# Performance work log

Hardware: AMD Instinct MI355X
Metric: run time of the kernel (lower is better)

## Reference

```python
import jax, jax.numpy as jnp
import numpy as np

C = 32        # channels after first 1x1 conv
HEADS = 4     # FuncSelfAttention heads ('channel' head split -> d = C // HEADS)


def setup_inputs() -> dict:
    key = jax.random.key(0)
    ks = jax.random.split(key, 8)
    B, H, W = 8, 512, 512
    s = 0.1
    return {
        "x": jax.random.normal(ks[0], (B, 1, H, W), jnp.float32),
        "n": 8,
        "m": 8,
        # Conv2d(1, C, kernel_size=1) == per-pixel linear 1->C
        "w1": jax.random.normal(ks[1], (C, 1), jnp.float32) * s,
        "b1": jax.random.normal(ks[2], (C,), jnp.float32) * s,
        # fused QKV projection over channels, bias=False
        "wqkv": jax.random.normal(ks[3], (3 * C, C), jnp.float32) * s,
        # output projection of the attention
        "wproj": jax.random.normal(ks[4], (C, C), jnp.float32) * s,
        "bproj": jax.random.normal(ks[5], (C,), jnp.float32) * s,
        # Conv2d(C, 1, kernel_size=1)
        "w2": jax.random.normal(ks[6], (1, C), jnp.float32) * s,
        "b2": jax.random.normal(ks[7], (1,), jnp.float32) * s,
    }


def reference(x, n, m, w1, b1, wqkv, wproj, bproj, w2, b2):
    B, _, H, W = x.shape
    d = C // HEADS
    hh, ww = H // n, W // m
    S, P = n * m, hh * ww  # subdomain tokens, quadrature points per token

    # 1x1 conv (pointwise linear over channel dim)
    h = jnp.einsum('oi,bihw->bohw', w1, x) + b1[None, :, None, None]

    # decompose2d: [B,C,H,W] -> [B, n*m, C, hh, ww] (flatten spatial per token)
    u = h.reshape(B, C, n, hh, m, ww).transpose(0, 2, 4, 1, 3, 5)
    u = u.reshape(B, S, C, P)

    # channel self-attention over subdomain functions
    qkv = jnp.einsum('oc,bscp->bsop', wqkv, u)          # [B,S,3C,P]
    q, k, v = jnp.split(qkv, 3, axis=2)
    q = q.reshape(B, S, HEADS, d, P)
    k = k.reshape(B, S, HEADS, d, P)
    v = v.reshape(B, S, HEADS, d, P)

    # L2 (quadrature-mean) inner product over points + head channels
    scale = 1.0 / (P * np.sqrt(d).astype(np.float32))
    scores = jnp.einsum('bihdp,bjhdp->bhij', q, k) * scale  # [B,H,S,S]
    attn = jax.nn.softmax(scores, axis=-1)
    o = jnp.einsum('bhij,bjhdp->bihdp', attn, v).reshape(B, S, C, P)
    o = jnp.einsum('oc,bscp->bsop', wproj, o) + bproj[None, None, :, None]

    # recompose2d: [B, n*m, C, hh, ww] -> [B, C, H, W]
    o = o.reshape(B, n, m, C, hh, ww).transpose(0, 3, 1, 4, 2, 5)
    o = o.reshape(B, C, H, W)

    # final 1x1 conv C -> 1
    out = jnp.einsum('oc,bchw->bohw', w2, o) + b2[None, :, None, None]
    return out
```

## Files before the change

kernel.cpp:

```cpp
#include <hip/hip_runtime.h>


#define CONST_OFF 0
#define SXP_OFF   16
#define WT_OFF    (16 + 128*64)
#define PART_OFF  (WT_OFF + 8*4096)

__global__ __launch_bounds__(256) void k1_gram(const float* __restrict__ x,
                                               float* __restrict__ ws)
{
    __shared__ float xs[64 * 68];
    int b = blockIdx.x >> 4, prg = blockIdx.x & 15;
    int t = threadIdx.x;
    const float* xb = x + (size_t)b * 262144;
    int tix = t & 15, tjx = t >> 4;

    float acc[4][4];
    #pragma unroll
    for (int u = 0; u < 4; ++u)
        #pragma unroll
        for (int v = 0; v < 4; ++v) acc[u][v] = 0.f;
    float tsum = 0.f;

    for (int it = 0; it < 4; ++it) {
        int pr = prg * 4 + it;
        __syncthreads();
        #pragma unroll
        for (int k = 0; k < 4; ++k) {
            int q = t + 256 * k;
            int tj = q >> 7, col4 = q & 127;
            float4 v = *(const float4*)(xb + (tj * 64 + pr) * 512 + col4 * 4);
            int token = tj * 8 + (col4 >> 4);
            *(float4*)(&xs[token * 68 + (col4 & 15) * 4]) = v;
        }
        __syncthreads();

        #pragma unroll 4
        for (int cq = 0; cq < 16; ++cq) {
            float4 a[4], bb[4];
            #pragma unroll
            for (int u = 0; u < 4; ++u)
                a[u] = *(const float4*)(&xs[(tix + 16 * u) * 68 + 4 * cq]);
            #pragma unroll
            for (int v = 0; v < 4; ++v)
                bb[v] = *(const float4*)(&xs[(tjx + 16 * v) * 68 + 4 * cq]);
            #pragma unroll
            for (int u = 0; u < 4; ++u)
                #pragma unroll
                for (int v = 0; v < 4; ++v)
                    acc[u][v] += a[u].x * bb[v].x + a[u].y * bb[v].y +
                                 a[u].z * bb[v].z + a[u].w * bb[v].w;
        }
        if (t < 64) {
            float s = 0.f;
            for (int c = 0; c < 64; ++c) s += xs[t * 68 + c];
            tsum += s;
        }
    }

    float* part = ws + PART_OFF + (size_t)blockIdx.x * 4096;
    #pragma unroll
    for (int u = 0; u < 4; ++u)
        #pragma unroll
        for (int v = 0; v < 4; ++v)
            part[(tix + 16 * u) * 64 + (tjx + 16 * v)] = acc[u][v];

    if (t < 64) ws[SXP_OFF + blockIdx.x * 64 + t] = tsum;
}

__global__ __launch_bounds__(1024) void k2_attn(
    const float* __restrict__ w1, const float* __restrict__ b1,
    const float* __restrict__ wqkv, const float* __restrict__ wproj,
    const float* __restrict__ bproj, const float* __restrict__ w2,
    const float* __restrict__ b2, float* __restrict__ ws)
{
    __shared__ float arow[96], crow[96], pvec[32];
    __shared__ float cst[16];
    __shared__ float G_s[64 * 65];
    __shared__ float sxp_s[16][64];
    __shared__ float sx_s[64];
    __shared__ float coef_s[4][64];
    __shared__ float m_s[4][64];
    int b = blockIdx.x, t = threadIdx.x;

    if (t < 96) {
        float sa = 0.f, sc = 0.f;
        for (int c = 0; c < 32; ++c) {
            float w = wqkv[t * 32 + c];
            sa += w * w1[c];
            sc += w * b1[c];
        }
        arow[t] = sa; crow[t] = sc;
    } else if (t < 128) {
        int c = t - 96;
        float s = 0.f;
        for (int oc = 0; oc < 32; ++oc) s += w2[oc] * wproj[oc * 32 + c];
        pvec[c] = s;
    }

    {
        const float* p0 = ws + PART_OFF + (size_t)(b * 16) * 4096 + t;
        float a0 = 0.f, a1 = 0.f, a2 = 0.f, a3 = 0.f;
        #pragma unroll
        for (int r = 0; r < 16; ++r) {
            const float* pr = p0 + (size_t)r * 4096;
            a0 += pr[0]; a1 += pr[1024]; a2 += pr[2048]; a3 += pr[3072];
        }
        int e0 = t;
        G_s[(e0 >> 6) * 65 + (e0 & 63)] = a0;
        int e1 = t + 1024;
        G_s[(e1 >> 6) * 65 + (e1 & 63)] = a1;
        int e2 = t + 2048;
        G_s[(e2 >> 6) * 65 + (e2 & 63)] = a2;
        int e3 = t + 3072;
        G_s[(e3 >> 6) * 65 + (e3 & 63)] = a3;
    }

    {
        int j = t & 63, rg = t >> 6;
        sxp_s[rg][j] = ws[SXP_OFF + (b * 16 + rg) * 64 + j];
    }
    __syncthreads();
    if (t < 64) {
        float s = 0.f;
        #pragma unroll
        for (int r = 0; r < 16; ++r) s += sxp_s[r][t];
        sx_s[t] = s;
    }

    const float scale = 1.0f / (4096.0f * 2.8284271247461903f);
    if (t >= 64 && t < 68) {
        int h = t - 64;
        float A = 0.f, Bk = 0.f, g = 0.f;
        #pragma unroll
        for (int dd = 0; dd < 8; ++dd) {
            int o = h * 8 + dd;
            A  += arow[o] * arow[32 + o];
            Bk += crow[o] * arow[32 + o];
            g  += pvec[o] * arow[64 + o];
        }
        cst[h]     = A * scale;
        cst[4 + h] = Bk * scale;
        cst[8 + h] = g;
    } else if (t == 68) {
        float c0 = b2[0];
        for (int c = 0; c < 32; ++c)  c0 += pvec[c] * crow[64 + c];
        for (int oc = 0; oc < 32; ++oc) c0 += w2[oc] * bproj[oc];
        cst[12] = c0;
    }
    __syncthreads();

    if (t < 256) {
        int h = t >> 6, i = t & 63;
        float A  = cst[h];
        float Bk = cst[4 + h];
        float g  = cst[8 + h];
        float m = -1e30f;
        for (int j = 0; j < 64; ++j) {
            float s = A * G_s[i * 65 + j] + Bk * sx_s[j];
            m = fmaxf(m, s);
        }
        float Z = 0.f;
        for (int j = 0; j < 64; ++j) {
            float s = A * G_s[i * 65 + j] + Bk * sx_s[j];
            Z += __expf(s - m);
        }
        coef_s[h][i] = g / Z;
        m_s[h][i]    = m;
    }
    __syncthreads();

    {
        float A0 = cst[0], A1 = cst[1], A2 = cst[2], A3 = cst[3];
        float B0 = cst[4], B1 = cst[5], B2 = cst[6], B3 = cst[7];
        #pragma unroll
        for (int k = 0; k < 4; ++k) {
            int e = t + 1024 * k;
            int j = e >> 6, i = e & 63;
            float G  = G_s[i * 65 + j];
            float sx = sx_s[j];
            float w =
                coef_s[0][i] * __expf(A0 * G + B0 * sx - m_s[0][i]) +
                coef_s[1][i] * __expf(A1 * G + B1 * sx - m_s[1][i]) +
                coef_s[2][i] * __expf(A2 * G + B2 * sx - m_s[2][i]) +
                coef_s[3][i] * __expf(A3 * G + B3 * sx - m_s[3][i]);
            ws[WT_OFF + b * 4096 + e] = w;
        }
    }
    if (b == 0 && t == 0) ws[CONST_OFF + 12] = cst[12];
}

__global__ __launch_bounds__(256) void k3_apply(const float* __restrict__ x,
                                                const float* __restrict__ ws,
                                                float* __restrict__ out)
{
    __shared__ float xs[64 * 68];
    __shared__ float Wt_s[64 * 68];
    int b = blockIdx.x >> 6, pr = blockIdx.x & 63;
    int t = threadIdx.x;
    const float* xb = x + (size_t)b * 262144;
    #pragma unroll
    for (int k = 0; k < 4; ++k) {
        int q = t + 256 * k;
        int tj = q >> 7, col4 = q & 127;
        float4 v = *(const float4*)(xb + (tj * 64 + pr) * 512 + col4 * 4);
        int token = tj * 8 + (col4 >> 4);
        *(float4*)(&xs[token * 68 + (col4 & 15) * 4]) = v;
        int j = q >> 4, i0 = (q & 15) * 4;
        float4 wv = *(const float4*)(ws + WT_OFF + b * 4096 + q * 4);
        *(float4*)(&Wt_s[j * 68 + i0]) = wv;
    }
    __syncthreads();

    int tcx = t & 15, tiy = t >> 4;
    float acc[4][4];
    #pragma unroll
    for (int u = 0; u < 4; ++u)
        #pragma unroll
        for (int v = 0; v < 4; ++v) acc[u][v] = 0.f;

    #pragma unroll 8
    for (int j = 0; j < 64; ++j) {
        float4 wv = *(const float4*)(&Wt_s[j * 68 + 4 * tiy]);
        float4 xv = *(const float4*)(&xs[j * 68 + 4 * tcx]);
        acc[0][0] += wv.x * xv.x; acc[0][1] += wv.x * xv.y;
        acc[0][2] += wv.x * xv.z; acc[0][3] += wv.x * xv.w;
        acc[1][0] += wv.y * xv.x; acc[1][1] += wv.y * xv.y;
        acc[1][2] += wv.y * xv.z; acc[1][3] += wv.y * xv.w;
        acc[2][0] += wv.z * xv.x; acc[2][1] += wv.z * xv.y;
        acc[2][2] += wv.z * xv.z; acc[2][3] += wv.z * xv.w;
        acc[3][0] += wv.w * xv.x; acc[3][1] += wv.w * xv.y;
        acc[3][2] += wv.w * xv.z; acc[3][3] += wv.w * xv.w;
    }

    float c0 = ws[CONST_OFF + 12];
    float* ob = out + (size_t)b * 262144;
    #pragma unroll
    for (int u = 0; u < 4; ++u) {
        int i = 4 * tiy + u;
        int ti = i >> 3, tk = i & 7;
        float4 r;
        r.x = acc[u][0] + c0; r.y = acc[u][1] + c0;
        r.z = acc[u][2] + c0; r.w = acc[u][3] + c0;
        *(float4*)(ob + (ti * 64 + pr) * 512 + tk * 64 + 4 * tcx) = r;
    }
}

extern "C" void kernel_launch(void* const* d_in, const int* in_sizes, int n_in,
                              void* d_out, int out_size, void* d_ws, size_t ws_size,
                              hipStream_t stream) {
    const float* x     = (const float*)d_in[0];
    const float* w1    = (const float*)d_in[3];
    const float* b1    = (const float*)d_in[4];
    const float* wqkv  = (const float*)d_in[5];
    const float* wproj = (const float*)d_in[6];
    const float* bproj = (const float*)d_in[7];
    const float* w2    = (const float*)d_in[8];
    const float* b2    = (const float*)d_in[9];
    float* out = (float*)d_out;
    float* ws  = (float*)d_ws;

    k1_gram<<<128, 256, 0, stream>>>(x, ws);
    k2_attn<<<8, 1024, 0, stream>>>(w1, b1, wqkv, wproj, bproj, w2, b2, ws);
    k3_apply<<<512, 256, 0, stream>>>(x, ws, out);
}
```

Measured before the change: 107.0 us.

## Compute per-token Gram matrix with bf16 MFMA instead of fp32 FMA

The Gram-matrix kernel now converts the input tile to bf16 in shared memory, loading all four row slices up front with a single barrier, and computes the 64x64 token Gram partials using 16x16x32 bf16 MFMA instructions instead of scalar fp32 dot products. The token sums are taken from the bf16 copy. This is meant to cut the ALU cost and the repeated LDS reads of the inner product loop. In exchange, input precision drops to bf16, which may hurt accuracy of the scores and row sums.

```diff
diff --git a/kernel.cpp b/kernel.cpp
--- a/kernel.cpp
+++ b/kernel.cpp
@@ -6,66 +6,77 @@
 #define WT_OFF    (16 + 128*64)
 #define PART_OFF  (WT_OFF + 8*4096)
 
+typedef __attribute__((ext_vector_type(8))) short bf16x8;
+typedef __attribute__((ext_vector_type(4))) float f32x4;
+
+__device__ __forceinline__ unsigned short f2bf(float f) {
+    unsigned int u = __float_as_uint(f);
+    u = (u + 0x7FFFu + ((u >> 16) & 1u)) >> 16;
+    return (unsigned short)u;
+}
+
 __global__ __launch_bounds__(256) void k1_gram(const float* __restrict__ x,
                                                float* __restrict__ ws)
 {
-    __shared__ float xs[64 * 68];
+    __shared__ unsigned short xsb[64 * 272];
     int b = blockIdx.x >> 4, prg = blockIdx.x & 15;
     int t = threadIdx.x;
     const float* xb = x + (size_t)b * 262144;
-    int tix = t & 15, tjx = t >> 4;
-
-    float acc[4][4];
-    #pragma unroll
-    for (int u = 0; u < 4; ++u)
-        #pragma unroll
-        for (int v = 0; v < 4; ++v) acc[u][v] = 0.f;
-    float tsum = 0.f;
-
-    for (int it = 0; it < 4; ++it) {
-        int pr = prg * 4 + it;
-        __syncthreads();
+
+    #pragma unroll
+    for (int prl = 0; prl < 4; ++prl) {
+        int pr = prg * 4 + prl;
         #pragma unroll
         for (int k = 0; k < 4; ++k) {
             int q = t + 256 * k;
             int tj = q >> 7, col4 = q & 127;
             float4 v = *(const float4*)(xb + (tj * 64 + pr) * 512 + col4 * 4);
             int token = tj * 8 + (col4 >> 4);
-            *(float4*)(&xs[token * 68 + (col4 & 15) * 4]) = v;
-        }
-        __syncthreads();
-
-        #pragma unroll 4
-        for (int cq = 0; cq < 16; ++cq) {
-            float4 a[4], bb[4];
-            #pragma unroll
-            for (int u = 0; u < 4; ++u)
-                a[u] = *(const float4*)(&xs[(tix + 16 * u) * 68 + 4 * cq]);
-            #pragma unroll
-            for (int v = 0; v < 4; ++v)
-                bb[v] = *(const float4*)(&xs[(tjx + 16 * v) * 68 + 4 * cq]);
-            #pragma unroll
-            for (int u = 0; u < 4; ++u)
-                #pragma unroll
-                for (int v = 0; v < 4; ++v)
-                    acc[u][v] += a[u].x * bb[v].x + a[u].y * bb[v].y +
-                                 a[u].z * bb[v].z + a[u].w * bb[v].w;
-        }
-        if (t < 64) {
-            float s = 0.f;
-            for (int c = 0; c < 64; ++c) s += xs[t * 68 + c];
-            tsum += s;
+            ushort4 h;
+            h.x = f2bf(v.x); h.y = f2bf(v.y); h.z = f2bf(v.z); h.w = f2bf(v.w);
+            *(ushort4*)(&xsb[token * 272 + prl * 64 + (col4 & 15) * 4]) = h;
+        }
+    }
+    __syncthreads();
+
+    if (t < 64) {
+        const uint4* p = (const uint4*)(&xsb[t * 272]);
+        float s = 0.f;
+        #pragma unroll
+        for (int c = 0; c < 32; ++c) {
+            uint4 u = p[c];
+            s += __uint_as_float(u.x << 16) + __uint_as_float(u.x & 0xFFFF0000u)
+               + __uint_as_float(u.y << 16) + __uint_as_float(u.y & 0xFFFF0000u)
+               + __uint_as_float(u.z << 16) + __uint_as_float(u.z & 0xFFFF0000u)
+               + __uint_as_float(u.w << 16) + __uint_as_float(u.w & 0xFFFF0000u);
+        }
+        ws[SXP_OFF + blockIdx.x * 64 + t] = s;
+    }
+
+    int w = t >> 6, lane = t & 63;
+    int m = lane & 15, quad = lane >> 4;
+    f32x4 acc[4];
+    #pragma unroll
+    for (int jq = 0; jq < 4; ++jq) acc[jq] = (f32x4){0.f, 0.f, 0.f, 0.f};
+
+    #pragma unroll
+    for (int s = 0; s < 8; ++s) {
+        int kb = s * 32 + quad * 8;
+        bf16x8 a = *(const bf16x8*)(&xsb[(w * 16 + m) * 272 + kb]);
+        #pragma unroll
+        for (int jq = 0; jq < 4; ++jq) {
+            bf16x8 bb = *(const bf16x8*)(&xsb[(jq * 16 + m) * 272 + kb]);
+            acc[jq] = __builtin_amdgcn_mfma_f32_16x16x32_bf16(a, bb, acc[jq],
+                                                              0, 0, 0);
         }
     }
 
     float* part = ws + PART_OFF + (size_t)blockIdx.x * 4096;
     #pragma unroll
-    for (int u = 0; u < 4; ++u)
-        #pragma unroll
-        for (int v = 0; v < 4; ++v)
-            part[(tix + 16 * u) * 64 + (tjx + 16 * v)] = acc[u][v];
-
-    if (t < 64) ws[SXP_OFF + blockIdx.x * 64 + t] = tsum;
+    for (int jq = 0; jq < 4; ++jq)
+        #pragma unroll
+        for (int r = 0; r < 4; ++r)
+            part[(w * 16 + quad * 4 + r) * 64 + jq * 16 + m] = acc[jq][r];
 }
 
 __global__ __launch_bounds__(1024) void k2_attn(
```

Measured after the change: 94.34 us. 1.13x faster.
